# Performance work log

Measured on AMD Instinct MI355X. Metric: run time of the kernel, lower is better.

The kernel has to match this reference:

```python
import jax, jax.numpy as jnp
import numpy as np

B, S, H, D, R = 2, 2048, 16, 128, 16
HID = H * D
ROPE_BASE = 10000.0


def _rotate_half(x):
    x1, x2 = x[..., : D // 2], x[..., D // 2:]
    return jnp.concatenate((-x2, x1), axis=-1)


def _sin_cos(position_ids):
    # full-dim RoPE (rope_fraction == 1)
    inv_freq = 1.0 / (ROPE_BASE ** (jnp.arange(0, D, 2, dtype=jnp.float32) / D))  # [D/2]
    freqs = position_ids.astype(jnp.float32)[..., None] * inv_freq  # [B,S,D/2]
    emb = jnp.concatenate((freqs, freqs), axis=-1)  # [B,S,D]
    # add head axis -> [B,1,S,D]
    return jnp.sin(emb)[:, None], jnp.cos(emb)[:, None]


def setup_inputs() -> dict:
    key = jax.random.key(0)
    ks = jax.random.split(key, 6)
    q = jax.random.normal(ks[0], (B, S, HID), dtype=jnp.float32)
    k = jax.random.normal(ks[1], (B, S, HID), dtype=jnp.float32)
    v = jax.random.normal(ks[2], (B, S, HID), dtype=jnp.float32)
    position_ids = jnp.tile(jnp.arange(S, dtype=jnp.int64)[None], (B, 1))
    causal = jnp.tril(jnp.ones((S, S), dtype=bool))
    attention_mask = jnp.where(causal, 0.0, -1e9).astype(jnp.float32)
    attention_mask = jnp.broadcast_to(attention_mask[None, None], (B, 1, S, S))
    k_registers = jax.random.normal(ks[3], (1, H, R, D), dtype=jnp.float32)
    v_registers = jax.random.normal(ks[4], (1, H, R, D), dtype=jnp.float32)
    return {
        "query_states": q,
        "key_states": k,
        "value_states": v,
        "position_ids": position_ids,
        "attention_mask": attention_mask,
        "k_registers": k_registers,
        "v_registers": v_registers,
    }


def reference(query_states, key_states, value_states, position_ids,
              attention_mask, k_registers, v_registers):
    bsz, q_len, _ = query_states.shape
    # [B,S,H*D] -> [B,H,S,D]
    q = query_states.reshape(bsz, q_len, H, D).transpose(0, 2, 1, 3)
    k = key_states.reshape(bsz, -1, H, D).transpose(0, 2, 1, 3)
    v = value_states.reshape(bsz, -1, H, D).transpose(0, 2, 1, 3)

    sin, cos = _sin_cos(position_ids)
    q = q * cos + _rotate_half(q) * sin
    k = k * cos + _rotate_half(k) * sin

    # concat learned register K/V tokens along kv-length
    k = jnp.concatenate((k, jnp.broadcast_to(k_registers, (bsz, H, R, D))), axis=2)
    v = jnp.concatenate((v, jnp.broadcast_to(v_registers, (bsz, H, R, D))), axis=2)
    mask = jnp.concatenate(
        (attention_mask,
         jnp.zeros(attention_mask.shape[:-1] + (R,), dtype=attention_mask.dtype)),
        axis=-1)

    scale = 1.0 / np.sqrt(D).astype(np.float32)
    scores = jnp.einsum('bhqd,bhkd->bhqk', q, k * scale) + mask  # [B,H,S,S+R]
    probs = jax.nn.softmax(scores.astype(jnp.float32), axis=-1).astype(q.dtype)
    out = jnp.einsum('bhqk,bhkd->bhqd', probs, v)
    return out.transpose(0, 2, 1, 3).reshape(bsz, q_len, H * D)
```

## Files before the change

### kernel.cpp

```cpp
#include <hip/hip_runtime.h>

#define S_LEN 2048
#define HID   2048
#define NH    16
#define HD    128
#define NREG  16
#define KPAD  2112
#define NBH   32

typedef float f32x4 __attribute__((ext_vector_type(4)));
typedef short s16x8 __attribute__((ext_vector_type(8)));

__device__ __forceinline__ unsigned short f2bf(float f) {
    union { float f; unsigned int u; } x; x.f = f;
    return (unsigned short)((x.u + 0x7FFFu + ((x.u >> 16) & 1u)) >> 16);
}
__device__ __forceinline__ unsigned short f2bf_t(float f) {
    union { float f; unsigned int u; } x; x.f = f;
    return (unsigned short)(x.u >> 16);
}
__device__ __forceinline__ void gl_lds16(const unsigned short* g, unsigned short* l) {
    __builtin_amdgcn_global_load_lds((const __attribute__((address_space(1))) void*)g,
                                     (__attribute__((address_space(3))) void*)l, 16, 0, 0);
}

__global__ void prepass_kernel(const float* __restrict__ k, const float* __restrict__ v,
                               const int* __restrict__ pos,
                               const float* __restrict__ kreg, const float* __restrict__ vreg,
                               unsigned short* __restrict__ Kb, unsigned short* __restrict__ Vt) {
    __shared__ unsigned short T[64][136];
    int bid = blockIdx.x, tid = threadIdx.x;

    if (bid < 4096) {
        int i  = bid * 256 + tid;
        int d4 = (i & 15) << 2;
        int h  = (i >> 4) & 15;
        int s  = (i >> 8) & 2047;
        int b  = i >> 19;
        float p = (float)pos[b * S_LEN + s];
        const float* kp = k + (size_t)(b * S_LEN + s) * HID + h * HD + d4;
        float4 k1 = *(const float4*)kp, k2 = *(const float4*)(kp + 64);
        const float* k1f = (const float*)&k1; const float* k2f = (const float*)&k2;
        unsigned short ok1[4], ok2[4];
        #pragma unroll
        for (int j = 0; j < 4; ++j) {
            float inv = exp2f((float)(d4 + j) * -0.20762050593046014f);
            float rev = p * inv * 0.15915494309189535f;
            rev -= rintf(rev);
            float a2 = rev * 6.283185307179586f;
            float sn = __sinf(a2), cs = __cosf(a2);
            ok1[j] = f2bf(k1f[j] * cs - k2f[j] * sn);
            ok2[j] = f2bf(k2f[j] * cs + k1f[j] * sn);
        }
        uint2 a;
        size_t ko = (size_t)((b * NH + h) * KPAD + s) * HD + d4;
        a.x = (unsigned)ok1[0] | ((unsigned)ok1[1] << 16);
        a.y = (unsigned)ok1[2] | ((unsigned)ok1[3] << 16);
        *(uint2*)(Kb + ko) = a;
        a.x = (unsigned)ok2[0] | ((unsigned)ok2[1] << 16);
        a.y = (unsigned)ok2[2] | ((unsigned)ok2[3] << 16);
        *(uint2*)(Kb + ko + 64) = a;
    } else if (bid < 5120) {
        int vb = bid - 4096;
        int tt = tid;
        int bh = vb >> 5, st = vb & 31;
        int b  = bh >> 4, h = bh & 15;
        {
            int key = tt >> 2, c = tt & 3;
            const float* src = v + (size_t)(b * S_LEN + st * 64 + key) * HID + h * HD;
            #pragma unroll
            for (int i = 0; i < 4; ++i) {
                int d0 = c * 32 + i * 8;
                float4 aa = *(const float4*)(src + d0);
                float4 bb = *(const float4*)(src + d0 + 4);
                unsigned short tmp[8] = { f2bf(aa.x), f2bf(aa.y), f2bf(aa.z), f2bf(aa.w),
                                          f2bf(bb.x), f2bf(bb.y), f2bf(bb.z), f2bf(bb.w) };
                *(uint4*)(&T[key][d0]) = *(const uint4*)tmp;
            }
        }
        __syncthreads();
        {
            int d = tt >> 1, half = tt & 1;
            unsigned short buf[32];
            #pragma unroll
            for (int i = 0; i < 32; ++i) buf[i] = T[half * 32 + i][d];
            uint4* dst = (uint4*)(Vt + ((size_t)(bh * HD + d)) * KPAD + st * 64 + half * 32);
            const uint4* bp = (const uint4*)buf;
            #pragma unroll
            for (int i = 0; i < 4; ++i) dst[i] = bp[i];
        }
    } else {
        int i = (bid - 5120) * 256 + tid;
        {
            int d = i & 127, r = (i >> 7) & 63, h = (i >> 13) & 15, b = i >> 17;
            float x = (r < NREG) ? kreg[(h * NREG + r) * HD + d] : 0.0f;
            Kb[((size_t)((b * NH + h) * KPAD + 2048 + r)) * HD + d] = f2bf(x);
        }
        {
            int r = i & 63, d = (i >> 6) & 127, h = (i >> 13) & 15, b = i >> 17;
            float x = (r < NREG) ? vreg[(h * NREG + r) * HD + d] : 0.0f;
            Vt[((size_t)((b * NH + h) * HD + d)) * KPAD + 2048 + r] = f2bf(x);
        }
    }
}

__global__ __launch_bounds__(256, 3)
void attn_kernel(const float* __restrict__ q, const int* __restrict__ pos,
                 const unsigned short* __restrict__ Kb,
                 const unsigned short* __restrict__ Vt, float* __restrict__ out) {
    __shared__ unsigned short Klds[64 * 128];
    __shared__ unsigned short Vtl[128 * 64];
    __shared__ unsigned short Plds[4 * 16 * 72];

    int idx = blockIdx.x;
    int bh  = idx & 31;
    int m   = 31 - (idx >> 5);
    int b = bh >> 4, h = bh & 15;
    int tid = threadIdx.x, w = tid >> 6, lane = tid & 63;
    int quad = lane >> 4, k15 = lane & 15;
    int s0q = m * 64;

    const unsigned short* kg[4]; unsigned short* klp[4];
    const unsigned short* vg[4]; unsigned short* vlp[4];
    {
        int krow = 16 * w + (lane >> 4);
        #pragma unroll
        for (int j = 0; j < 4; ++j) {
            int key = krow + 4 * j;
            kg[j]  = Kb + ((size_t)bh * KPAD + key) * HD + (((lane & 15) ^ (key & 15)) << 3);
            klp[j] = Klds + (16 * w + 4 * j) * HD;
        }
        int drow = 32 * w + (lane >> 3);
        int vsw  = ((lane & 7) ^ (lane >> 3)) << 3;
        #pragma unroll
        for (int j = 0; j < 4; ++j) {
            vg[j]  = Vt + ((size_t)bh * HD + drow + 8 * j) * KPAD + vsw;
            vlp[j] = Vtl + (32 * w + 8 * j) * 64;
        }
    }

    s16x8 qa[4];
    {
        int row = s0q + w * 16 + k15;
        float p = (float)pos[b * S_LEN + row];
        const float* qp = q + (size_t)(b * S_LEN + row) * HID + h * HD + quad * 8;
        #pragma unroll
        for (int kc = 0; kc < 2; ++kc) {
            float4 xa = *(const float4*)(qp + kc * 32);
            float4 xb = *(const float4*)(qp + kc * 32 + 4);
            float4 ya = *(const float4*)(qp + kc * 32 + 64);
            float4 yb = *(const float4*)(qp + kc * 32 + 68);
            float x1[8] = {xa.x, xa.y, xa.z, xa.w, xb.x, xb.y, xb.z, xb.w};
            float x2[8] = {ya.x, ya.y, ya.z, ya.w, yb.x, yb.y, yb.z, yb.w};
            unsigned short lo[8], hi[8];
            #pragma unroll
            for (int j = 0; j < 8; ++j) {
                int dh = kc * 32 + quad * 8 + j;
                float inv = exp2f((float)dh * -0.20762050593046014f);
                float rev = p * inv * 0.15915494309189535f;
                rev -= rintf(rev);
                float a2 = rev * 6.283185307179586f;
                float sn = __sinf(a2), cs = __cosf(a2);
                const float scale = 0.08838834764831845f;
                lo[j] = f2bf((x1[j] * cs - x2[j] * sn) * scale);
                hi[j] = f2bf((x2[j] * cs + x1[j] * sn) * scale);
            }
            qa[kc]     = *(const s16x8*)lo;
            qa[kc + 2] = *(const s16x8*)hi;
        }
    }

    f32x4 oacc[8];
    float lsum[4];
    #pragma unroll
    for (int nc = 0; nc < 8; ++nc) oacc[nc] = (f32x4){0.f, 0.f, 0.f, 0.f};
    #pragma unroll
    for (int r = 0; r < 4; ++r) lsum[r] = 0.f;

    auto stage = [&](int kbase) {
        size_t ko = (size_t)kbase * HD;
        #pragma unroll
        for (int j = 0; j < 4; ++j) gl_lds16(kg[j] + ko, klp[j]);
        #pragma unroll
        for (int j = 0; j < 4; ++j) gl_lds16(vg[j] + kbase, vlp[j]);
    };

    auto tile = [&](int mode) {
        f32x4 sc[4];
        #pragma unroll
        for (int nc = 0; nc < 4; ++nc) {
            sc[nc] = (f32x4){0.f, 0.f, 0.f, 0.f};
            if (mode == 2 && nc > 0) continue;
            #pragma unroll
            for (int kc = 0; kc < 4; ++kc) {
                const s16x8 bf = *(const s16x8*)(Klds + (nc * 16 + k15) * HD +
                                                 (((4 * kc + quad) ^ k15) << 3));
                sc[nc] = __builtin_amdgcn_mfma_f32_16x16x32_bf16(qa[kc], bf, sc[nc], 0, 0, 0);
            }
        }
        int rowb = w * 16 + quad * 4;
        #pragma unroll
        for (int r = 0; r < 4; ++r) {
            float p[4];
            #pragma unroll
            for (int nc = 0; nc < 4; ++nc) {
                if (mode == 2 && nc > 0) { p[nc] = 0.f; continue; }
                float e = __expf(sc[nc][r]);
                bool valid = (mode != 1) || (nc * 16 + k15 <= rowb + r);
                p[nc] = valid ? e : 0.f;
            }
            lsum[r] += (p[0] + p[1]) + (p[2] + p[3]);
            int prow = w * (16 * 72) + (quad * 4 + r) * 72 + k15;
            Plds[prow]      = f2bf_t(p[0]);
            Plds[prow + 16] = f2bf_t(p[1]);
            Plds[prow + 32] = f2bf_t(p[2]);
            Plds[prow + 48] = f2bf_t(p[3]);
        }
        #pragma unroll
        for (int kc = 0; kc < 2; ++kc) {
            if (mode == 2 && kc > 0) continue;
            const s16x8 pf = *(const s16x8*)(Plds + w * (16 * 72) + k15 * 72 +
                                             kc * 32 + quad * 8);
            #pragma unroll
            for (int nc = 0; nc < 8; ++nc) {
                const s16x8 vf = *(const s16x8*)(Vtl + (nc * 16 + k15) * 64 +
                                                 (((4 * kc + quad) ^ (k15 & 7)) << 3));
                oacc[nc] = __builtin_amdgcn_mfma_f32_16x16x32_bf16(pf, vf, oacc[nc], 0, 0, 0);
            }
        }
    };

    for (int kt = 0; kt < m; ++kt) {
        __syncthreads();
        stage(kt * 64);
        __syncthreads();
        tile(0);
    }
    __syncthreads();
    stage(m * 64);
    __syncthreads();
    tile(1);
    __syncthreads();
    stage(2048);
    __syncthreads();
    tile(2);

    #pragma unroll
    for (int r = 0; r < 4; ++r) {
        float lv = lsum[r];
        #pragma unroll
        for (int off = 1; off < 16; off <<= 1) lv += __shfl_xor(lv, off);
        float invl = 1.0f / lv;
        size_t row = (size_t)(b * S_LEN + s0q + w * 16 + quad * 4 + r) * HID
                     + h * HD + k15;
        #pragma unroll
        for (int nc = 0; nc < 8; ++nc)
            out[row + nc * 16] = oacc[nc][r] * invl;
    }
}

extern "C" void kernel_launch(void* const* d_in, const int* in_sizes, int n_in,
                              void* d_out, int out_size, void* d_ws, size_t ws_size,
                              hipStream_t stream) {
    const float* q    = (const float*)d_in[0];
    const float* k    = (const float*)d_in[1];
    const float* v    = (const float*)d_in[2];
    const int*   pos  = (const int*)d_in[3];
    const float* kreg = (const float*)d_in[5];
    const float* vreg = (const float*)d_in[6];
    float* out = (float*)d_out;

    unsigned short* Kb = (unsigned short*)d_ws;
    unsigned short* Vt = Kb + (size_t)NBH * KPAD * HD;

    prepass_kernel<<<dim3(6144), dim3(256), 0, stream>>>(k, v, pos, kreg, vreg, Kb, Vt);
    attn_kernel<<<dim3(1024), dim3(256), 0, stream>>>(q, pos, Kb, Vt, out);
}
```

Baseline: 211.3 us.

## Double-buffer K/V LDS tiles to overlap async loads with MFMA compute

```diff
diff --git a/kernel.cpp b/kernel.cpp
--- a/kernel.cpp
+++ b/kernel.cpp
@@ -104,12 +104,12 @@
     }
 }
 
-__global__ __launch_bounds__(256, 3)
+__global__ __launch_bounds__(256, 2)
 void attn_kernel(const float* __restrict__ q, const int* __restrict__ pos,
                  const unsigned short* __restrict__ Kb,
                  const unsigned short* __restrict__ Vt, float* __restrict__ out) {
-    __shared__ unsigned short Klds[64 * 128];
-    __shared__ unsigned short Vtl[128 * 64];
+    __shared__ unsigned short Klds[2 * 64 * 128];
+    __shared__ unsigned short Vtl[2 * 128 * 64];
     __shared__ unsigned short Plds[4 * 16 * 72];
 
     int idx = blockIdx.x;
@@ -138,6 +138,16 @@
             vlp[j] = Vtl + (32 * w + 8 * j) * 64;
         }
     }
+    auto stage = [&](int kbase, int buf) {
+        size_t ko = (size_t)kbase * HD;
+        int off = buf * 8192;
+        #pragma unroll
+        for (int j = 0; j < 4; ++j) gl_lds16(kg[j] + ko, klp[j] + off);
+        #pragma unroll
+        for (int j = 0; j < 4; ++j) gl_lds16(vg[j] + kbase, vlp[j] + off);
+    };
+
+    stage(0, 0);
 
     s16x8 qa[4];
     {
@@ -177,15 +187,9 @@
     #pragma unroll
     for (int r = 0; r < 4; ++r) lsum[r] = 0.f;
 
-    auto stage = [&](int kbase) {
-        size_t ko = (size_t)kbase * HD;
-        #pragma unroll
-        for (int j = 0; j < 4; ++j) gl_lds16(kg[j] + ko, klp[j]);
-        #pragma unroll
-        for (int j = 0; j < 4; ++j) gl_lds16(vg[j] + kbase, vlp[j]);
-    };
-
-    auto tile = [&](int mode) {
+    auto tile = [&](int mode, int buf) {
+        const unsigned short* Kc = Klds + buf * 8192;
+        const unsigned short* Vc = Vtl + buf * 8192;
         f32x4 sc[4];
         #pragma unroll
         for (int nc = 0; nc < 4; ++nc) {
@@ -193,7 +197,7 @@
             if (mode == 2 && nc > 0) continue;
             #pragma unroll
             for (int kc = 0; kc < 4; ++kc) {
-                const s16x8 bf = *(const s16x8*)(Klds + (nc * 16 + k15) * HD +
+                const s16x8 bf = *(const s16x8*)(Kc + (nc * 16 + k15) * HD +
                                                  (((4 * kc + quad) ^ k15) << 3));
                 sc[nc] = __builtin_amdgcn_mfma_f32_16x16x32_bf16(qa[kc], bf, sc[nc], 0, 0, 0);
             }
@@ -223,27 +227,28 @@
                                              kc * 32 + quad * 8);
             #pragma unroll
             for (int nc = 0; nc < 8; ++nc) {
-                const s16x8 vf = *(const s16x8*)(Vtl + (nc * 16 + k15) * 64 +
+                const s16x8 vf = *(const s16x8*)(Vc + (nc * 16 + k15) * 64 +
                                                  (((4 * kc + quad) ^ (k15 & 7)) << 3));
                 oacc[nc] = __builtin_amdgcn_mfma_f32_16x16x32_bf16(pf, vf, oacc[nc], 0, 0, 0);
             }
         }
     };
 
-    for (int kt = 0; kt < m; ++kt) {
+    __syncthreads();
+
+    int cur = 0;
+    int NT  = m + 2;
+    #pragma unroll 1
+    for (int kt = 0; kt < NT; ++kt) {
+        int  mode = (kt < m) ? 0 : ((kt == m) ? 1 : 2);
+        bool more = (kt + 1 < NT);
+        int  nkb  = (kt + 1 <= m) ? (kt + 1) * 64 : 2048;
+
+        if (more) stage(nkb, cur ^ 1);
+        tile(mode, cur);
         __syncthreads();
-        stage(kt * 64);
-        __syncthreads();
-        tile(0);
-    }
-    __syncthreads();
-    stage(m * 64);
-    __syncthreads();
-    tile(1);
-    __syncthreads();
-    stage(2048);
-    __syncthreads();
-    tile(2);
+        cur ^= 1;
+    }
 
     #pragma unroll
     for (int r = 0; r < 4; ++r) {
```

Result: slower. 223.4 us (+5.7%).

## Switch attention to 32x32 MFMA with 128-row query tiles and register-resident P

Applied to the files above, without the earlier changes.

```diff
diff --git a/kernel.cpp b/kernel.cpp
--- a/kernel.cpp
+++ b/kernel.cpp
@@ -8,20 +8,23 @@
 #define KPAD  2112
 #define NBH   32
 
-typedef float f32x4 __attribute__((ext_vector_type(4)));
-typedef short s16x8 __attribute__((ext_vector_type(8)));
+typedef float f32x4  __attribute__((ext_vector_type(4)));
+typedef float f32x16 __attribute__((ext_vector_type(16)));
+typedef short s16x8  __attribute__((ext_vector_type(8)));
 
 __device__ __forceinline__ unsigned short f2bf(float f) {
     union { float f; unsigned int u; } x; x.f = f;
     return (unsigned short)((x.u + 0x7FFFu + ((x.u >> 16) & 1u)) >> 16);
 }
-__device__ __forceinline__ unsigned short f2bf_t(float f) {
-    union { float f; unsigned int u; } x; x.f = f;
-    return (unsigned short)(x.u >> 16);
-}
 __device__ __forceinline__ void gl_lds16(const unsigned short* g, unsigned short* l) {
     __builtin_amdgcn_global_load_lds((const __attribute__((address_space(1))) void*)g,
                                      (__attribute__((address_space(3))) void*)l, 16, 0, 0);
+}
+__device__ __forceinline__ f32x16 zero16() {
+    f32x16 z;
+    #pragma unroll
+    for (int i = 0; i < 16; ++i) z[i] = 0.f;
+    return z;
 }
 
 __global__ void prepass_kernel(const float* __restrict__ k, const float* __restrict__ v,
@@ -104,21 +107,22 @@
     }
 }
 
-__global__ __launch_bounds__(256, 3)
+__global__ __launch_bounds__(256, 2)
 void attn_kernel(const float* __restrict__ q, const int* __restrict__ pos,
                  const unsigned short* __restrict__ Kb,
                  const unsigned short* __restrict__ Vt, float* __restrict__ out) {
     __shared__ unsigned short Klds[64 * 128];
     __shared__ unsigned short Vtl[128 * 64];
-    __shared__ unsigned short Plds[4 * 16 * 72];
 
     int idx = blockIdx.x;
     int bh  = idx & 31;
-    int m   = 31 - (idx >> 5);
+    int j5  = idx >> 5;
+    int t   = (idx < 256) ? (15 - 2 * j5) : (2 * (j5 - 8));
     int b = bh >> 4, h = bh & 15;
     int tid = threadIdx.x, w = tid >> 6, lane = tid & 63;
-    int quad = lane >> 4, k15 = lane & 15;
-    int s0q = m * 64;
+    int l31 = lane & 31, hi = lane >> 5;
+    int s0q = t * 128;
+    int qrel = 32 * w + l31;
 
     const unsigned short* kg[4]; unsigned short* klp[4];
     const unsigned short* vg[4]; unsigned short* vlp[4];
@@ -138,125 +142,152 @@
             vlp[j] = Vtl + (32 * w + 8 * j) * 64;
         }
     }
-
-    s16x8 qa[4];
+    auto stage = [&](int kbase) {
+        size_t ko = (size_t)kbase * HD;
+        #pragma unroll
+        for (int j = 0; j < 4; ++j) gl_lds16(kg[j] + ko, klp[j]);
+        #pragma unroll
+        for (int j = 0; j < 4; ++j) gl_lds16(vg[j] + kbase, vlp[j]);
+    };
+
+    stage(0);
+
+    s16x8 qb[8];
     {
-        int row = s0q + w * 16 + k15;
+        int row = s0q + qrel;
         float p = (float)pos[b * S_LEN + row];
-        const float* qp = q + (size_t)(b * S_LEN + row) * HID + h * HD + quad * 8;
-        #pragma unroll
-        for (int kc = 0; kc < 2; ++kc) {
-            float4 xa = *(const float4*)(qp + kc * 32);
-            float4 xb = *(const float4*)(qp + kc * 32 + 4);
-            float4 ya = *(const float4*)(qp + kc * 32 + 64);
-            float4 yb = *(const float4*)(qp + kc * 32 + 68);
+        const float* qp = q + (size_t)(b * S_LEN + row) * HID + h * HD + hi * 8;
+        #pragma unroll
+        for (int kc = 0; kc < 4; ++kc) {
+            float4 xa = *(const float4*)(qp + 16 * kc);
+            float4 xb = *(const float4*)(qp + 16 * kc + 4);
+            float4 ya = *(const float4*)(qp + 16 * kc + 64);
+            float4 yb = *(const float4*)(qp + 16 * kc + 68);
             float x1[8] = {xa.x, xa.y, xa.z, xa.w, xb.x, xb.y, xb.z, xb.w};
             float x2[8] = {ya.x, ya.y, ya.z, ya.w, yb.x, yb.y, yb.z, yb.w};
-            unsigned short lo[8], hi[8];
+            unsigned short lo[8], hh[8];
             #pragma unroll
             for (int j = 0; j < 8; ++j) {
-                int dh = kc * 32 + quad * 8 + j;
+                int dh = 16 * kc + hi * 8 + j;
                 float inv = exp2f((float)dh * -0.20762050593046014f);
                 float rev = p * inv * 0.15915494309189535f;
                 rev -= rintf(rev);
                 float a2 = rev * 6.283185307179586f;
                 float sn = __sinf(a2), cs = __cosf(a2);
-                const float scale = 0.08838834764831845f;
+                const float scale = 0.12751744610657577f;
                 lo[j] = f2bf((x1[j] * cs - x2[j] * sn) * scale);
-                hi[j] = f2bf((x2[j] * cs + x1[j] * sn) * scale);
-            }
-            qa[kc]     = *(const s16x8*)lo;
-            qa[kc + 2] = *(const s16x8*)hi;
+                hh[j] = f2bf((x2[j] * cs + x1[j] * sn) * scale);
+            }
+            qb[kc]     = *(const s16x8*)lo;
+            qb[kc + 4] = *(const s16x8*)hh;
         }
     }
 
-    f32x4 oacc[8];
-    float lsum[4];
+    f32x16 od[4];
     #pragma unroll
-    for (int nc = 0; nc < 8; ++nc) oacc[nc] = (f32x4){0.f, 0.f, 0.f, 0.f};
+    for (int dt = 0; dt < 4; ++dt) od[dt] = zero16();
+    float lsum = 0.f;
+
+    auto kread = [&](int mt, int kc) -> s16x8 {
+        int row = 32 * mt + l31;
+        int g   = (hi + 2 * kc) ^ (lane & 15);
+        return *(const s16x8*)(Klds + row * 128 + g * 8);
+    };
+    auto vread = [&](int dt, int ks) -> s16x8 {
+        int row = 32 * dt + l31;
+        int g   = (hi + 2 * ks) ^ (lane & 7);
+        return *(const s16x8*)(Vtl + row * 64 + g * 8);
+    };
+
+    auto smpack = [&](const f32x16& sc, int mt, int mode, int coff, s16x8* pa) {
+        float p[16];
+        #pragma unroll
+        for (int reg = 0; reg < 16; ++reg) {
+            float e = exp2f(sc[reg]);
+            if (mode == 1) {
+                int crow = (reg & 3) + 8 * (reg >> 2);
+                bool valid = (coff + 32 * mt + crow + 4 * hi) <= qrel;
+                e = valid ? e : 0.f;
+            }
+            if (mode == 2 && reg >= 8) e = 0.f;
+            p[reg] = e;
+        }
+        lsum += (((p[0] + p[1]) + (p[2] + p[3])) + ((p[4] + p[5]) + (p[6] + p[7])))
+              + (((p[8] + p[9]) + (p[10] + p[11])) + ((p[12] + p[13]) + (p[14] + p[15])));
+        int nkk = (mode == 2) ? 1 : 2;
+        #pragma unroll
+        for (int kk = 0; kk < 2; ++kk) {
+            if (kk >= nkk) continue;
+            int base = 8 * kk;
+            unsigned pk0, pk1, pk2, pk3;
+            asm("v_cvt_pk_bf16_f32 %0, %1, %2" : "=v"(pk0) : "v"(p[base + 0]), "v"(p[base + 1]));
+            asm("v_cvt_pk_bf16_f32 %0, %1, %2" : "=v"(pk1) : "v"(p[base + 2]), "v"(p[base + 3]));
+            asm("v_cvt_pk_bf16_f32 %0, %1, %2" : "=v"(pk2) : "v"(p[base + 4]), "v"(p[base + 5]));
+            asm("v_cvt_pk_bf16_f32 %0, %1, %2" : "=v"(pk3) : "v"(p[base + 6]), "v"(p[base + 7]));
+            asm("v_permlane32_swap_b32 %0, %1" : "+v"(pk0), "+v"(pk2));
+            asm("v_permlane32_swap_b32 %0, %1" : "+v"(pk1), "+v"(pk3));
+            union { s16x8 v; unsigned u[4]; } pw;
+            pw.u[0] = pk0; pw.u[1] = pk1; pw.u[2] = pk2; pw.u[3] = pk3;
+            pa[kk] = pw.v;
+        }
+    };
+
+    __syncthreads();
+
+    int NT = 2 * t + 3;
+    #pragma unroll 1
+    for (int kt = 0; kt < NT; ++kt) {
+        int mode, coff = 0;
+        bool skip = false;
+        if (kt < 2 * t)            mode = 0;
+        else if (kt == 2 * t)      mode = (w >= 2) ? 0 : 1;
+        else if (kt == 2 * t + 1) { coff = 64; if (w < 2) skip = true; mode = 1; }
+        else                       mode = 2;
+
+        if (!skip) {
+            f32x16 sA = zero16(), sB = zero16();
+            #pragma unroll
+            for (int kc = 0; kc < 8; ++kc) {
+                sA = __builtin_amdgcn_mfma_f32_32x32x16_bf16(kread(0, kc), qb[kc], sA, 0, 0, 0);
+                if (mode != 2)
+                    sB = __builtin_amdgcn_mfma_f32_32x32x16_bf16(kread(1, kc), qb[kc], sB, 0, 0, 0);
+            }
+            s16x8 pa[4];
+            smpack(sA, 0, mode, coff, &pa[0]);
+            if (mode != 2) smpack(sB, 1, mode, coff, &pa[2]);
+            int nks = (mode == 2) ? 1 : 4;
+            #pragma unroll
+            for (int ks = 0; ks < 4; ++ks) {
+                if (ks >= nks) continue;
+                #pragma unroll
+                for (int dt = 0; dt < 4; ++dt)
+                    od[dt] = __builtin_amdgcn_mfma_f32_32x32x16_bf16(vread(dt, ks), pa[ks],
+                                                                     od[dt], 0, 0, 0);
+            }
+        }
+
+        __syncthreads();
+        if (kt + 1 < NT) {
+            int nkb = (kt + 1 <= 2 * t + 1) ? (kt + 1) * 64 : 2048;
+            stage(nkb);
+            __syncthreads();
+        }
+    }
+
+    float lv = lsum + __shfl_xor(lsum, 32);
+    float invl = 1.0f / lv;
+    size_t rowbase = (size_t)(b * S_LEN + s0q + qrel) * HID + h * HD;
     #pragma unroll
-    for (int r = 0; r < 4; ++r) lsum[r] = 0.f;
-
-    auto stage = [&](int kbase) {
-        size_t ko = (size_t)kbase * HD;
-        #pragma unroll
-        for (int j = 0; j < 4; ++j) gl_lds16(kg[j] + ko, klp[j]);
-        #pragma unroll
-        for (int j = 0; j < 4; ++j) gl_lds16(vg[j] + kbase, vlp[j]);
-    };
-
-    auto tile = [&](int mode) {
-        f32x4 sc[4];
-        #pragma unroll
-        for (int nc = 0; nc < 4; ++nc) {
-            sc[nc] = (f32x4){0.f, 0.f, 0.f, 0.f};
-            if (mode == 2 && nc > 0) continue;
-            #pragma unroll
-            for (int kc = 0; kc < 4; ++kc) {
-                const s16x8 bf = *(const s16x8*)(Klds + (nc * 16 + k15) * HD +
-                                                 (((4 * kc + quad) ^ k15) << 3));
-                sc[nc] = __builtin_amdgcn_mfma_f32_16x16x32_bf16(qa[kc], bf, sc[nc], 0, 0, 0);
-            }
-        }
-        int rowb = w * 16 + quad * 4;
-        #pragma unroll
-        for (int r = 0; r < 4; ++r) {
-            float p[4];
-            #pragma unroll
-            for (int nc = 0; nc < 4; ++nc) {
-                if (mode == 2 && nc > 0) { p[nc] = 0.f; continue; }
-                float e = __expf(sc[nc][r]);
-                bool valid = (mode != 1) || (nc * 16 + k15 <= rowb + r);
-                p[nc] = valid ? e : 0.f;
-            }
-            lsum[r] += (p[0] + p[1]) + (p[2] + p[3]);
-            int prow = w * (16 * 72) + (quad * 4 + r) * 72 + k15;
-            Plds[prow]      = f2bf_t(p[0]);
-            Plds[prow + 16] = f2bf_t(p[1]);
-            Plds[prow + 32] = f2bf_t(p[2]);
-            Plds[prow + 48] = f2bf_t(p[3]);
-        }
-        #pragma unroll
-        for (int kc = 0; kc < 2; ++kc) {
-            if (mode == 2 && kc > 0) continue;
-            const s16x8 pf = *(const s16x8*)(Plds + w * (16 * 72) + k15 * 72 +
-                                             kc * 32 + quad * 8);
-            #pragma unroll
-            for (int nc = 0; nc < 8; ++nc) {
-                const s16x8 vf = *(const s16x8*)(Vtl + (nc * 16 + k15) * 64 +
-                                                 (((4 * kc + quad) ^ (k15 & 7)) << 3));
-                oacc[nc] = __builtin_amdgcn_mfma_f32_16x16x32_bf16(pf, vf, oacc[nc], 0, 0, 0);
-            }
-        }
-    };
-
-    for (int kt = 0; kt < m; ++kt) {
-        __syncthreads();
-        stage(kt * 64);
-        __syncthreads();
-        tile(0);
-    }
-    __syncthreads();
-    stage(m * 64);
-    __syncthreads();
-    tile(1);
-    __syncthreads();
-    stage(2048);
-    __syncthreads();
-    tile(2);
-
-    #pragma unroll
-    for (int r = 0; r < 4; ++r) {
-        float lv = lsum[r];
-        #pragma unroll
-        for (int off = 1; off < 16; off <<= 1) lv += __shfl_xor(lv, off);
-        float invl = 1.0f / lv;
-        size_t row = (size_t)(b * S_LEN + s0q + w * 16 + quad * 4 + r) * HID
-                     + h * HD + k15;
-        #pragma unroll
-        for (int nc = 0; nc < 8; ++nc)
-            out[row + nc * 16] = oacc[nc][r] * invl;
-    }
+    for (int dt = 0; dt < 4; ++dt)
+        #pragma unroll
+        for (int rq = 0; rq < 4; ++rq) {
+            float4 o;
+            o.x = od[dt][4 * rq + 0] * invl;
+            o.y = od[dt][4 * rq + 1] * invl;
+            o.z = od[dt][4 * rq + 2] * invl;
+            o.w = od[dt][4 * rq + 3] * invl;
+            *(float4*)(out + rowbase + 32 * dt + 8 * rq + 4 * hi) = o;
+        }
 }
 
 extern "C" void kernel_launch(void* const* d_in, const int* in_sizes, int n_in,
@@ -274,5 +305,5 @@
     unsigned short* Vt = Kb + (size_t)NBH * KPAD * HD;
 
     prepass_kernel<<<dim3(6144), dim3(256), 0, stream>>>(k, v, pos, kreg, vreg, Kb, Vt);
-    attn_kernel<<<dim3(1024), dim3(256), 0, stream>>>(q, pos, Kb, Vt, out);
-}
+    attn_kernel<<<dim3(512), dim3(256), 0, stream>>>(q, pos, Kb, Vt, out);
+}
```

Result: slower. 251.3 us (+18.9%).
